# Performance work log

Measured on AMD Instinct MI355X. Metric: run time of the kernel, lower is better.

## Reference

```python
import jax, jax.numpy as jnp
import numpy as np

R = 16
SEQ_LEN = 96
D_MODEL = 512
D_FF = 2048


def tr_linear(x2d, in_cores, out_cores, bias):
    # Tensor-ring linear: W[i1..im, o1..on] = Tr(G1[i1]...Gm[im] H1[o1]...Hn[on])
    # y = x @ W.reshape(prod(in), prod(out)) + bias, computed without forming W fully.
    b = x2d.shape[0]
    in_dims = tuple(c.shape[1] for c in in_cores)
    t = x2d.reshape((b,) + in_dims)
    # fold input modes into the ring: s ends as [b, r0, r_m]
    s = jnp.tensordot(t, in_cores[0], axes=[[1], [1]])  # [b, i2..im, r0, r1]
    for core in in_cores[1:]:
        s = jnp.einsum('bi...ac,cid->b...ad', s, core)
    # fold output cores into W: [r_m, o1..on, r0]
    W = out_cores[0]
    for core in out_cores[1:]:
        W = jnp.einsum('c...d,dpe->c...pe', W, core)
    # close the ring: trace over (r0, r_m)
    y = jnp.einsum('bac,c...a->b...', s, W)
    return y.reshape(b, -1) + bias


def ffn_forward(x, c1_in2, c1_in3, c1_ind, c1_out_seq, c1_out_ff, b1,
                c2_in_seq, c2_in_ff, c2_out2, c2_out3, c2_outd, b2):
    B, L, D = x.shape
    in1 = list(c1_in2) + [c1_in3, c1_ind]          # factorint(96)+[d_model] modes
    out1 = [c1_out_seq, c1_out_ff]                 # [seq_len, d_ff]
    h = tr_linear(x.reshape(B, L * D), in1, out1, b1)   # [B, seq_len*d_ff]
    h = jax.nn.relu(h)                             # dropout = identity (eval mode)
    in2 = [c2_in_seq, c2_in_ff]
    out2 = list(c2_out2) + [c2_out3, c2_outd]
    y = tr_linear(h, in2, out2, b2)                # [B, seq_len*d_model]
    return y.reshape(B, L, D)                      # output.view(x.shape)


def setup_inputs():
    key = jax.random.key(0)
    ks = jax.random.split(key, 13)
    s = 0.2  # core init scale keeps 9-core ring products near unit magnitude
    return {
        'x': jax.random.normal(ks[0], (64, SEQ_LEN, D_MODEL), jnp.float32),
        'c1_in2': s * jax.random.normal(ks[1], (5, R, 2, R), jnp.float32),
        'c1_in3': s * jax.random.normal(ks[2], (R, 3, R), jnp.float32),
        'c1_ind': s * jax.random.normal(ks[3], (R, D_MODEL, R), jnp.float32),
        'c1_out_seq': s * jax.random.normal(ks[4], (R, SEQ_LEN, R), jnp.float32),
        'c1_out_ff': s * jax.random.normal(ks[5], (R, D_FF, R), jnp.float32),
        'b1': 0.01 * jax.random.normal(ks[6], (SEQ_LEN * D_FF,), jnp.float32),
        'c2_in_seq': s * jax.random.normal(ks[7], (R, SEQ_LEN, R), jnp.float32),
        'c2_in_ff': s * jax.random.normal(ks[8], (R, D_FF, R), jnp.float32),
        'c2_out2': s * jax.random.normal(ks[9], (5, R, 2, R), jnp.float32),
        'c2_out3': s * jax.random.normal(ks[10], (R, 3, R), jnp.float32),
        'c2_outd': s * jax.random.normal(ks[11], (R, D_MODEL, R), jnp.float32),
        'b2': 0.01 * jax.random.normal(ks[12], (SEQ_LEN * D_MODEL,), jnp.float32),
    }


def reference(x, c1_in2, c1_in3, c1_ind, c1_out_seq, c1_out_ff, b1,
              c2_in_seq, c2_in_ff, c2_out2, c2_out3, c2_outd, b2):
    return ffn_forward(x, c1_in2, c1_in3, c1_ind, c1_out_seq, c1_out_ff, b1,
                       c2_in_seq, c2_in_ff, c2_out2, c2_out3, c2_outd, b2)
```

## Files before the change

### kernel.cpp

```cpp
#include <hip/hip_runtime.h>


typedef _Float16 f16;
typedef f16 f16x8 __attribute__((ext_vector_type(8)));
typedef f16 f16x4 __attribute__((ext_vector_type(4)));
typedef float f32x4 __attribute__((ext_vector_type(4)));

__global__ void build_chain_kernel(
    const float* __restrict__ a5, const float* __restrict__ a3,
    const float* __restrict__ b5, const float* __restrict__ b3,
    float* __restrict__ Pout, float* __restrict__ Qout)
{
    __shared__ float bufA[8192];
    __shared__ float bufB[4096];
    const float* cores5 = (blockIdx.x == 0) ? a5 : b5;
    const float* core3  = (blockIdx.x == 0) ? a3 : b3;
    float* out = (blockIdx.x == 0) ? Pout : Qout;
    const int tid = threadIdx.x;

    for (int i = tid; i < 512; i += 256) bufA[i] = cores5[i];
    __syncthreads();

    float* prev = bufA; float* next = bufB;
    int m = 2;
    for (int g = 1; g < 5; ++g) {
        const float* G = cores5 + g * 512;
        const int mnew = m * 2;
        const int total = 256 * mnew;
        for (int idx = tid; idx < total; idx += 256) {
            const int rn = idx & 15;
            const int mm = (idx >> 4) % mnew;
            const int r0 = idx / (mnew * 16);
            const int mp = mm >> 1, i = mm & 1;
            float acc = 0.f;
            #pragma unroll
            for (int r = 0; r < 16; ++r)
                acc += prev[(r0 * m + mp) * 16 + r] * G[r * 32 + i * 16 + rn];
            next[idx] = acc;
        }
        __syncthreads();
        float* t = prev; prev = next; next = t;
        m = mnew;
    }
    {
        const int mnew = m * 3;
        const int total = 256 * mnew;
        for (int idx = tid; idx < total; idx += 256) {
            const int rn = idx & 15;
            const int mm = (idx >> 4) % mnew;
            const int r0 = idx / (mnew * 16);
            const int mp = mm / 3, i = mm % 3;
            float acc = 0.f;
            #pragma unroll
            for (int r = 0; r < 16; ++r)
                acc += prev[(r0 * m + mp) * 16 + r] * core3[r * 48 + i * 16 + rn];
            out[idx] = acc;
        }
    }
}

__global__ void permM_kernel(const float* __restrict__ in, f16* __restrict__ bh,
                             f16* __restrict__ bl, int K) {
    __shared__ float t[4096];
    const int q = blockIdx.x, k0 = blockIdx.y * 256;
    const float* src = in + ((size_t)q * K + k0) * 16;
    for (int i = threadIdx.x; i < 1024; i += 256)
        ((float4*)t)[i] = ((const float4*)src)[i];
    __syncthreads();
    const int j = threadIdx.x >> 4, kc = (threadIdx.x & 15) * 16;
    f16* dh = bh + (size_t)(q * 16 + j) * K + k0 + kc;
    f16* dl = bl + (size_t)(q * 16 + j) * K + k0 + kc;
    f16 vh[16], vl[16];
    #pragma unroll
    for (int i = 0; i < 16; ++i) {
        const float v = t[(kc + i) * 16 + j];
        const f16 h = (f16)v;
        vh[i] = h; vl[i] = (f16)(v - (float)h);
    }
    *(f16x8*)(dh) = *(f16x8*)&vh[0]; *(f16x8*)(dh + 8) = *(f16x8*)&vh[8];
    *(f16x8*)(dl) = *(f16x8*)&vl[0]; *(f16x8*)(dl + 8) = *(f16x8*)&vl[8];
}
__global__ void permO_kernel(const float* __restrict__ in, f16* __restrict__ bh,
                             f16* __restrict__ bl, int N) {
    const int idx = blockIdx.x * 256 + threadIdx.x;
    const int n = idx >> 8, k = idx & 255;
    const float v = in[((k >> 4) * N + n) * 16 + (k & 15)];
    const f16 h = (f16)v;
    bh[idx] = h; bl[idx] = (f16)(v - (float)h);
}

__global__ void xsplit_kernel(const float* __restrict__ x, f16* __restrict__ xh,
                              f16* __restrict__ xl) {
    const int idx = blockIdx.x * 256 + threadIdx.x;
    const float4 v = ((const float4*)x)[idx];
    f16x4 hh, ll;
    hh[0] = (f16)v.x; hh[1] = (f16)v.y; hh[2] = (f16)v.z; hh[3] = (f16)v.w;
    ll[0] = (f16)(v.x - (float)hh[0]); ll[1] = (f16)(v.y - (float)hh[1]);
    ll[2] = (f16)(v.z - (float)hh[2]); ll[3] = (f16)(v.w - (float)hh[3]);
    ((f16x4*)xh)[idx] = hh; ((f16x4*)xl)[idx] = ll;
}

__global__ void sfold_kernel(const float* __restrict__ z, const float* __restrict__ P,
                             float* __restrict__ spart, int SK) {
    const int b = blockIdx.x, lc = blockIdx.y, tid = threadIdx.x;
    const int r0 = tid >> 4, rE = tid & 15;
    float acc = 0.f;
    for (int sk = 0; sk < SK; ++sk) {
        const float* zb = z + ((size_t)sk * 6144 + b * 96) * 256;
        for (int l = lc * 16; l < lc * 16 + 16; ++l) {
            const float* zl = zb + l * 256 + rE;
            const float* Pl = P + (r0 * 96 + l) * 16;
            #pragma unroll
            for (int r = 0; r < 16; ++r) acc += zl[r * 16] * Pl[r];
        }
    }
    spart[((size_t)lc * 64 + b) * 256 + tid] = acc;
}

__global__ void uexpand_kernel(const float* __restrict__ spart, const float* __restrict__ O,
                               f16* __restrict__ uh, f16* __restrict__ ul) {
    __shared__ float s_sh[256], o_sh[256];
    const int o1 = blockIdx.x, b = blockIdx.y, tid = threadIdx.x;
    float sv = 0.f;
    #pragma unroll
    for (int lc = 0; lc < 6; ++lc) sv += spart[((size_t)lc * 64 + b) * 256 + tid];
    s_sh[tid] = sv;
    o_sh[tid] = O[((tid >> 4) * 96 + o1) * 16 + (tid & 15)];
    __syncthreads();
    const int dd = tid >> 4, a = tid & 15;
    float acc = 0.f;
    #pragma unroll
    for (int c = 0; c < 16; ++c) acc += s_sh[a * 16 + c] * o_sh[c * 16 + dd];
    const f16 h = (f16)acc;
    const size_t o = ((size_t)b * 96 + o1) * 256 + tid;
    uh[o] = h; ul[o] = (f16)(acc - (float)h);
}

template<int EPI>
__global__ __launch_bounds__(256) void trgemm_kernel(
    const f16* __restrict__ Ah, const f16* __restrict__ Al,
    const f16* __restrict__ BTh, const f16* __restrict__ BTl,
    const float* __restrict__ bias,
    float* __restrict__ Cf, f16* __restrict__ Ch, f16* __restrict__ Cl,
    int M, int N, int K, int kchunk)
{
    __shared__ f16 As[2][4 * 512];
    __shared__ f16 Bs[2][8 * 512];
    const int n0 = blockIdx.x * 128, m0 = blockIdx.y * 64;
    const int kbase = blockIdx.z * kchunk;
    const int tid = threadIdx.x;
    const int w = tid >> 6, lane = tid & 63;

    const int ar = tid >> 2, aq = tid & 3;
    const int bn = tid >> 1, bsg = tid & 1;
    const size_t a_off = (size_t)(m0 + ar) * K + kbase + aq * 8;
    const size_t b_off = (size_t)(n0 + bn) * K + kbase + bsg * 16;
    const int a_w = (ar >> 4) * 512 + aq * 128 + (ar & 15) * 8;
    const int b_w = (bn >> 4) * 512 + (bsg * 2) * 128 + (bn & 15) * 8;

    f32x4 acc[4][2];
    #pragma unroll
    for (int i = 0; i < 4; ++i) { acc[i][0] = (f32x4)0.f; acc[i][1] = (f32x4)0.f; }

    const int nkt = kchunk >> 5;
    for (int kt = 0; kt < nkt; ++kt) {
        const size_t ao = a_off + (size_t)kt * 32;
        const size_t bo = b_off + (size_t)kt * 32;
        const f16x8 avh = *(const f16x8*)(Ah + ao);
        const f16x8 avl = *(const f16x8*)(Al + ao);
        const f16x8 bvh0 = *(const f16x8*)(BTh + bo);
        const f16x8 bvh1 = *(const f16x8*)(BTh + bo + 8);
        const f16x8 bvl0 = *(const f16x8*)(BTl + bo);
        const f16x8 bvl1 = *(const f16x8*)(BTl + bo + 8);
        __syncthreads();
        *(f16x8*)&As[0][a_w] = avh;
        *(f16x8*)&As[1][a_w] = avl;
        *(f16x8*)&Bs[0][b_w] = bvh0;
        *(f16x8*)&Bs[0][b_w + 128] = bvh1;
        *(f16x8*)&Bs[1][b_w] = bvl0;
        *(f16x8*)&Bs[1][b_w + 128] = bvl1;
        __syncthreads();
        f16x8 afh[4], afl[4], bfh[2], bfl[2];
        #pragma unroll
        for (int mf = 0; mf < 4; ++mf) {
            afh[mf] = *(const f16x8*)&As[0][mf * 512 + lane * 8];
            afl[mf] = *(const f16x8*)&As[1][mf * 512 + lane * 8];
        }
        #pragma unroll
        for (int nf = 0; nf < 2; ++nf) {
            bfh[nf] = *(const f16x8*)&Bs[0][(w * 2 + nf) * 512 + lane * 8];
            bfl[nf] = *(const f16x8*)&Bs[1][(w * 2 + nf) * 512 + lane * 8];
        }
        #pragma unroll
        for (int mf = 0; mf < 4; ++mf)
            #pragma unroll
            for (int nf = 0; nf < 2; ++nf) {
                acc[mf][nf] = __builtin_amdgcn_mfma_f32_16x16x32_f16(afh[mf], bfh[nf], acc[mf][nf], 0, 0, 0);
                acc[mf][nf] = __builtin_amdgcn_mfma_f32_16x16x32_f16(afh[mf], bfl[nf], acc[mf][nf], 0, 0, 0);
                acc[mf][nf] = __builtin_amdgcn_mfma_f32_16x16x32_f16(afl[mf], bfh[nf], acc[mf][nf], 0, 0, 0);
            }
    }

    const int g = lane >> 4, c = lane & 15;
    #pragma unroll
    for (int mf = 0; mf < 4; ++mf)
        #pragma unroll
        for (int nf = 0; nf < 2; ++nf)
            #pragma unroll
            for (int r = 0; r < 4; ++r) {
                const int row = m0 + mf * 16 + g * 4 + r;
                const int col = n0 + w * 32 + nf * 16 + c;
                float v = acc[mf][nf][r];
                if constexpr (EPI == 0) {
                    Cf[((size_t)blockIdx.z * M + row) * N + col] = v;
                } else {
                    v += bias[(row % 96) * N + col];
                    if constexpr (EPI == 1) {
                        v = fmaxf(v, 0.f);
                        const f16 h = (f16)v;
                        Ch[(size_t)row * N + col] = h;
                        Cl[(size_t)row * N + col] = (f16)(v - (float)h);
                    } else {
                        Cf[(size_t)row * N + col] = v;
                    }
                }
            }
}

extern "C" void kernel_launch(void* const* d_in, const int* in_sizes, int n_in,
                              void* d_out, int out_size, void* d_ws, size_t ws_size,
                              hipStream_t stream) {
    const float* x        = (const float*)d_in[0];
    const float* c1_in2   = (const float*)d_in[1];
    const float* c1_in3   = (const float*)d_in[2];
    const float* c1_ind   = (const float*)d_in[3];
    const float* c1_oseq  = (const float*)d_in[4];
    const float* c1_off   = (const float*)d_in[5];
    const float* b1       = (const float*)d_in[6];
    const float* c2_iseq  = (const float*)d_in[7];
    const float* c2_iff   = (const float*)d_in[8];
    const float* c2_out2  = (const float*)d_in[9];
    const float* c2_out3  = (const float*)d_in[10];
    const float* c2_outd  = (const float*)d_in[11];
    const float* b2       = (const float*)d_in[12];
    float* out = (float*)d_out;

    float* wsf = (float*)d_ws;
    float* Pseq1 = wsf;
    float* Qseq2 = Pseq1 + 24576;
    float* spart = Qseq2 + 24576;
    float* zp    = spart + 98304;
    f16* fb   = (f16*)(zp + 2 * 6144 * 256);
    f16* BT1h = fb;
    f16* BT1l = BT1h + 131072;
    f16* BT2h = BT1l + 131072;
    f16* BT2l = BT2h + 524288;
    f16* BT3h = BT2l + 524288;
    f16* BT3l = BT3h + 524288;
    f16* BT4h = BT3l + 524288;
    f16* BT4l = BT4h + 131072;
    f16* uh   = BT4l + 131072;
    f16* ul   = uh + 1572864;
    f16* hh   = ul + 1572864;
    f16* hl   = hh + 12582912;
    f16* xh   = hh;
    f16* xl   = hh + 3145728;

    build_chain_kernel<<<2, 256, 0, stream>>>(c1_in2, c1_in3, c2_out2, c2_out3, Pseq1, Qseq2);
    permM_kernel<<<dim3(16, 2), 256, 0, stream>>>(c1_ind, BT1h, BT1l, 512);
    permO_kernel<<<2048, 256, 0, stream>>>(c1_off, BT2h, BT2l, 2048);
    permM_kernel<<<dim3(16, 8), 256, 0, stream>>>(c2_iff, BT3h, BT3l, 2048);
    permO_kernel<<<512, 256, 0, stream>>>(c2_outd, BT4h, BT4l, 512);
    xsplit_kernel<<<3072, 256, 0, stream>>>(x, xh, xl);

    trgemm_kernel<0><<<dim3(2, 96, 2), 256, 0, stream>>>(xh, xl, BT1h, BT1l, nullptr,
                                                         zp, nullptr, nullptr, 6144, 256, 512, 256);
    sfold_kernel<<<dim3(64, 6), 256, 0, stream>>>(zp, Pseq1, spart, 2);
    uexpand_kernel<<<dim3(96, 64), 256, 0, stream>>>(spart, c1_oseq, uh, ul);
    trgemm_kernel<1><<<dim3(16, 96, 1), 256, 0, stream>>>(uh, ul, BT2h, BT2l, b1,
                                                          nullptr, hh, hl, 6144, 2048, 256, 256);
    trgemm_kernel<0><<<dim3(2, 96, 2), 256, 0, stream>>>(hh, hl, BT3h, BT3l, nullptr,
                                                         zp, nullptr, nullptr, 6144, 256, 2048, 1024);
    sfold_kernel<<<dim3(64, 6), 256, 0, stream>>>(zp, c2_iseq, spart, 2);
    uexpand_kernel<<<dim3(96, 64), 256, 0, stream>>>(spart, Qseq2, uh, ul);
    trgemm_kernel<2><<<dim3(4, 96, 1), 256, 0, stream>>>(uh, ul, BT4h, BT4l, b2,
                                                         out, nullptr, nullptr, 6144, 512, 256, 256);
}
```

Before: 270.5 us.

## Rework TR-FFN pipeline: larger GEMM tiles, direct LDS loads, fused prep kernels

The GEMM moves from 64x128 to 128x128 block tiles with a 64-wide k step, loads tiles with global_load_lds straight into shared memory, and declares launch bounds of 256 threads with 2 blocks per CU. The chain-building kernel is parallelised across 192 blocks (one per sequence index) instead of 2. The four weight-permute kernels are merged into one launch. sfold now stages z and P in shared memory. Split-K rises to 4 when the workspace is large enough. Larger tiles give each block more data reuse but also launch fewer blocks and raise register and LDS pressure.

```diff
diff --git a/kernel.cpp b/kernel.cpp
--- a/kernel.cpp
+++ b/kernel.cpp
@@ -6,63 +6,45 @@
 typedef f16 f16x4 __attribute__((ext_vector_type(4)));
 typedef float f32x4 __attribute__((ext_vector_type(4)));
 
-__global__ void build_chain_kernel(
-    const float* __restrict__ a5, const float* __restrict__ a3,
-    const float* __restrict__ b5, const float* __restrict__ b3,
-    float* __restrict__ Pout, float* __restrict__ Qout)
-{
-    __shared__ float bufA[8192];
-    __shared__ float bufB[4096];
-    const float* cores5 = (blockIdx.x == 0) ? a5 : b5;
-    const float* core3  = (blockIdx.x == 0) ? a3 : b3;
-    float* out = (blockIdx.x == 0) ? Pout : Qout;
-    const int tid = threadIdx.x;
-
-    for (int i = tid; i < 512; i += 256) bufA[i] = cores5[i];
+__device__ __forceinline__ void gload16(const void* g, void* l) {
+    __builtin_amdgcn_global_load_lds(
+        (const __attribute__((address_space(1))) void*)g,
+        (__attribute__((address_space(3))) void*)l, 16, 0, 0);
+}
+
+__global__ void build_chain2_kernel(const float* __restrict__ a5, const float* __restrict__ a3,
+                                    const float* __restrict__ b5, const float* __restrict__ b3,
+                                    float* __restrict__ Pout, float* __restrict__ Qout) {
+    __shared__ float Ma[256], Mb[256];
+    const int l = blockIdx.x % 96, chain = blockIdx.x / 96;
+    const float* G5 = chain ? b5 : a5;
+    const float* G3 = chain ? b3 : a3;
+    float* out = chain ? Qout : Pout;
+    const int i6 = l % 3, lh = l / 3;
+    const int dig[5] = {(lh >> 4) & 1, (lh >> 3) & 1, (lh >> 2) & 1, (lh >> 1) & 1, lh & 1};
+    const int a = threadIdx.x >> 4, bn = threadIdx.x & 15;
+    Ma[threadIdx.x] = G5[a * 32 + dig[0] * 16 + bn];
     __syncthreads();
-
-    float* prev = bufA; float* next = bufB;
-    int m = 2;
+    float* cur = Ma; float* nxt = Mb;
     for (int g = 1; g < 5; ++g) {
-        const float* G = cores5 + g * 512;
-        const int mnew = m * 2;
-        const int total = 256 * mnew;
-        for (int idx = tid; idx < total; idx += 256) {
-            const int rn = idx & 15;
-            const int mm = (idx >> 4) % mnew;
-            const int r0 = idx / (mnew * 16);
-            const int mp = mm >> 1, i = mm & 1;
-            float acc = 0.f;
-            #pragma unroll
-            for (int r = 0; r < 16; ++r)
-                acc += prev[(r0 * m + mp) * 16 + r] * G[r * 32 + i * 16 + rn];
-            next[idx] = acc;
-        }
-        __syncthreads();
-        float* t = prev; prev = next; next = t;
-        m = mnew;
-    }
-    {
-        const int mnew = m * 3;
-        const int total = 256 * mnew;
-        for (int idx = tid; idx < total; idx += 256) {
-            const int rn = idx & 15;
-            const int mm = (idx >> 4) % mnew;
-            const int r0 = idx / (mnew * 16);
-            const int mp = mm / 3, i = mm % 3;
-            float acc = 0.f;
-            #pragma unroll
-            for (int r = 0; r < 16; ++r)
-                acc += prev[(r0 * m + mp) * 16 + r] * core3[r * 48 + i * 16 + rn];
-            out[idx] = acc;
-        }
-    }
-}
-
-__global__ void permM_kernel(const float* __restrict__ in, f16* __restrict__ bh,
-                             f16* __restrict__ bl, int K) {
-    __shared__ float t[4096];
-    const int q = blockIdx.x, k0 = blockIdx.y * 256;
+        float s = 0.f;
+        #pragma unroll
+        for (int r = 0; r < 16; ++r)
+            s += cur[a * 16 + r] * G5[g * 512 + r * 32 + dig[g] * 16 + bn];
+        nxt[threadIdx.x] = s;
+        __syncthreads();
+        float* t = cur; cur = nxt; nxt = t;
+    }
+    float s = 0.f;
+    #pragma unroll
+    for (int r = 0; r < 16; ++r)
+        s += cur[a * 16 + r] * G3[r * 48 + i6 * 16 + bn];
+    out[(a * 96 + l) * 16 + bn] = s;
+}
+
+__device__ __forceinline__ void permM_body(const float* __restrict__ in, f16* __restrict__ bh,
+                                           f16* __restrict__ bl, int K, int q, int k0,
+                                           float* t) {
     const float* src = in + ((size_t)q * K + k0) * 16;
     for (int i = threadIdx.x; i < 1024; i += 256)
         ((float4*)t)[i] = ((const float4*)src)[i];
@@ -80,13 +62,27 @@
     *(f16x8*)(dh) = *(f16x8*)&vh[0]; *(f16x8*)(dh + 8) = *(f16x8*)&vh[8];
     *(f16x8*)(dl) = *(f16x8*)&vl[0]; *(f16x8*)(dl + 8) = *(f16x8*)&vl[8];
 }
-__global__ void permO_kernel(const float* __restrict__ in, f16* __restrict__ bh,
-                             f16* __restrict__ bl, int N) {
-    const int idx = blockIdx.x * 256 + threadIdx.x;
+__device__ __forceinline__ void permO_body(const float* __restrict__ in, f16* __restrict__ bh,
+                                           f16* __restrict__ bl, int N, int blk) {
+    const int idx = blk * 256 + threadIdx.x;
     const int n = idx >> 8, k = idx & 255;
     const float v = in[((k >> 4) * N + n) * 16 + (k & 15)];
     const f16 h = (f16)v;
     bh[idx] = h; bl[idx] = (f16)(v - (float)h);
+}
+__global__ void prep_bt_kernel(const float* __restrict__ c1_ind, const float* __restrict__ c1_off,
+                               const float* __restrict__ c2_iff, const float* __restrict__ c2_outd,
+                               f16* BT1h, f16* BT1l, f16* BT2h, f16* BT2l,
+                               f16* BT3h, f16* BT3l, f16* BT4h, f16* BT4l) {
+    __shared__ float t[4096];
+    int b = blockIdx.x;
+    if (b < 32)   { permM_body(c1_ind, BT1h, BT1l, 512,  b & 15, (b >> 4) * 256, t); return; }
+    b -= 32;
+    if (b < 128)  { permM_body(c2_iff, BT3h, BT3l, 2048, b & 15, (b >> 4) * 256, t); return; }
+    b -= 128;
+    if (b < 2048) { permO_body(c1_off, BT2h, BT2l, 2048, b); return; }
+    b -= 2048;
+    permO_body(c2_outd, BT4h, BT4l, 512, b);
 }
 
 __global__ void xsplit_kernel(const float* __restrict__ x, f16* __restrict__ xh,
@@ -102,17 +98,25 @@
 
 __global__ void sfold_kernel(const float* __restrict__ z, const float* __restrict__ P,
                              float* __restrict__ spart, int SK) {
+    __shared__ float zs[4096];
+    __shared__ float Ps[4096];
     const int b = blockIdx.x, lc = blockIdx.y, tid = threadIdx.x;
     const int r0 = tid >> 4, rE = tid & 15;
+    for (int i = tid; i < 4096; i += 256) {
+        const int rp = i & 15, r = (i >> 4) & 15, l = i >> 8;
+        Ps[i] = P[((size_t)rp * 96 + lc * 16 + l) * 16 + r];
+    }
     float acc = 0.f;
     for (int sk = 0; sk < SK; ++sk) {
-        const float* zb = z + ((size_t)sk * 6144 + b * 96) * 256;
-        for (int l = lc * 16; l < lc * 16 + 16; ++l) {
-            const float* zl = zb + l * 256 + rE;
-            const float* Pl = P + (r0 * 96 + l) * 16;
-            #pragma unroll
-            for (int r = 0; r < 16; ++r) acc += zl[r * 16] * Pl[r];
-        }
+        const float4* zsrc = (const float4*)(z + ((size_t)sk * 6144 + b * 96 + lc * 16) * 256);
+        __syncthreads();
+        for (int i = tid; i < 1024; i += 256) ((float4*)zs)[i] = zsrc[i];
+        __syncthreads();
+        #pragma unroll
+        for (int l = 0; l < 16; ++l)
+            #pragma unroll
+            for (int r = 0; r < 16; ++r)
+                acc += zs[l * 256 + r * 16 + rE] * Ps[(l * 16 + r) * 16 + r0];
     }
     spart[((size_t)lc * 64 + b) * 256 + tid] = acc;
 }
@@ -137,84 +141,87 @@
 }
 
 template<int EPI>
-__global__ __launch_bounds__(256) void trgemm_kernel(
+__global__ __launch_bounds__(256, 2) void trgemm_kernel(
     const f16* __restrict__ Ah, const f16* __restrict__ Al,
     const f16* __restrict__ BTh, const f16* __restrict__ BTl,
     const float* __restrict__ bias,
     float* __restrict__ Cf, f16* __restrict__ Ch, f16* __restrict__ Cl,
     int M, int N, int K, int kchunk)
 {
-    __shared__ f16 As[2][4 * 512];
-    __shared__ f16 Bs[2][8 * 512];
-    const int n0 = blockIdx.x * 128, m0 = blockIdx.y * 64;
+    __shared__ f16 As[2][8192];
+    __shared__ f16 Bs[2][8192];
+    const int n0 = blockIdx.x * 128, m0 = blockIdx.y * 128;
     const int kbase = blockIdx.z * kchunk;
     const int tid = threadIdx.x;
     const int w = tid >> 6, lane = tid & 63;
-
-    const int ar = tid >> 2, aq = tid & 3;
-    const int bn = tid >> 1, bsg = tid & 1;
-    const size_t a_off = (size_t)(m0 + ar) * K + kbase + aq * 8;
-    const size_t b_off = (size_t)(n0 + bn) * K + kbase + bsg * 16;
-    const int a_w = (ar >> 4) * 512 + aq * 128 + (ar & 15) * 8;
-    const int b_w = (bn >> 4) * 512 + (bsg * 2) * 128 + (bn & 15) * 8;
-
-    f32x4 acc[4][2];
-    #pragma unroll
-    for (int i = 0; i < 4; ++i) { acc[i][0] = (f32x4)0.f; acc[i][1] = (f32x4)0.f; }
-
-    const int nkt = kchunk >> 5;
+    const int wm = w >> 1, wn = w & 1;
+    const int lr = lane & 15, lq = lane >> 4;
+
+    const int ra = 2 * w;
+    size_t aoff0 = (size_t)(m0 + ra * 16 + lr) * K + kbase + lq * 8;
+    size_t aoff1 = aoff0 + (size_t)16 * K;
+    size_t boff0 = (size_t)(n0 + ra * 16 + lr) * K + kbase + lq * 8;
+    size_t boff1 = boff0 + (size_t)16 * K;
+
+    f32x4 acc[4][4];
+    #pragma unroll
+    for (int i = 0; i < 4; ++i)
+        #pragma unroll
+        for (int j = 0; j < 4; ++j) acc[i][j] = (f32x4)0.f;
+
+    const int nkt = kchunk >> 6;
     for (int kt = 0; kt < nkt; ++kt) {
-        const size_t ao = a_off + (size_t)kt * 32;
-        const size_t bo = b_off + (size_t)kt * 32;
-        const f16x8 avh = *(const f16x8*)(Ah + ao);
-        const f16x8 avl = *(const f16x8*)(Al + ao);
-        const f16x8 bvh0 = *(const f16x8*)(BTh + bo);
-        const f16x8 bvh1 = *(const f16x8*)(BTh + bo + 8);
-        const f16x8 bvl0 = *(const f16x8*)(BTl + bo);
-        const f16x8 bvl1 = *(const f16x8*)(BTl + bo + 8);
-        __syncthreads();
-        *(f16x8*)&As[0][a_w] = avh;
-        *(f16x8*)&As[1][a_w] = avl;
-        *(f16x8*)&Bs[0][b_w] = bvh0;
-        *(f16x8*)&Bs[0][b_w + 128] = bvh1;
-        *(f16x8*)&Bs[1][b_w] = bvl0;
-        *(f16x8*)&Bs[1][b_w + 128] = bvl1;
-        __syncthreads();
-        f16x8 afh[4], afl[4], bfh[2], bfl[2];
-        #pragma unroll
-        for (int mf = 0; mf < 4; ++mf) {
-            afh[mf] = *(const f16x8*)&As[0][mf * 512 + lane * 8];
-            afl[mf] = *(const f16x8*)&As[1][mf * 512 + lane * 8];
+        __syncthreads();
+        #pragma unroll
+        for (int c = 0; c < 2; ++c) {
+            gload16(Ah + aoff0 + c * 32, &As[0][(ra + 0) * 1024 + c * 512]);
+            gload16(Ah + aoff1 + c * 32, &As[0][(ra + 1) * 1024 + c * 512]);
+            gload16(Al + aoff0 + c * 32, &As[1][(ra + 0) * 1024 + c * 512]);
+            gload16(Al + aoff1 + c * 32, &As[1][(ra + 1) * 1024 + c * 512]);
+            gload16(BTh + boff0 + c * 32, &Bs[0][(ra + 0) * 1024 + c * 512]);
+            gload16(BTh + boff1 + c * 32, &Bs[0][(ra + 1) * 1024 + c * 512]);
+            gload16(BTl + boff0 + c * 32, &Bs[1][(ra + 0) * 1024 + c * 512]);
+            gload16(BTl + boff1 + c * 32, &Bs[1][(ra + 1) * 1024 + c * 512]);
         }
-        #pragma unroll
-        for (int nf = 0; nf < 2; ++nf) {
-            bfh[nf] = *(const f16x8*)&Bs[0][(w * 2 + nf) * 512 + lane * 8];
-            bfl[nf] = *(const f16x8*)&Bs[1][(w * 2 + nf) * 512 + lane * 8];
+        aoff0 += 64; aoff1 += 64; boff0 += 64; boff1 += 64;
+        __syncthreads();
+        #pragma unroll
+        for (int ks = 0; ks < 2; ++ks) {
+            f16x8 afh[4], afl[4], bfh[4], bfl[4];
+            #pragma unroll
+            for (int mf = 0; mf < 4; ++mf) {
+                afh[mf] = *(const f16x8*)&As[0][(wm * 4 + mf) * 1024 + ks * 512 + lane * 8];
+                afl[mf] = *(const f16x8*)&As[1][(wm * 4 + mf) * 1024 + ks * 512 + lane * 8];
+            }
+            #pragma unroll
+            for (int nf = 0; nf < 4; ++nf) {
+                bfh[nf] = *(const f16x8*)&Bs[0][(wn * 4 + nf) * 1024 + ks * 512 + lane * 8];
+                bfl[nf] = *(const f16x8*)&Bs[1][(wn * 4 + nf) * 1024 + ks * 512 + lane * 8];
+            }
+            #pragma unroll
+            for (int mf = 0; mf < 4; ++mf)
+                #pragma unroll
+                for (int nf = 0; nf < 4; ++nf) {
+                    acc[mf][nf] = __builtin_amdgcn_mfma_f32_16x16x32_f16(afh[mf], bfh[nf], acc[mf][nf], 0, 0, 0);
+                    acc[mf][nf] = __builtin_amdgcn_mfma_f32_16x16x32_f16(afh[mf], bfl[nf], acc[mf][nf], 0, 0, 0);
+                    acc[mf][nf] = __builtin_amdgcn_mfma_f32_16x16x32_f16(afl[mf], bfh[nf], acc[mf][nf], 0, 0, 0);
+                }
         }
-        #pragma unroll
-        for (int mf = 0; mf < 4; ++mf)
-            #pragma unroll
-            for (int nf = 0; nf < 2; ++nf) {
-                acc[mf][nf] = __builtin_amdgcn_mfma_f32_16x16x32_f16(afh[mf], bfh[nf], acc[mf][nf], 0, 0, 0);
-                acc[mf][nf] = __builtin_amdgcn_mfma_f32_16x16x32_f16(afh[mf], bfl[nf], acc[mf][nf], 0, 0, 0);
-                acc[mf][nf] = __builtin_amdgcn_mfma_f32_16x16x32_f16(afl[mf], bfh[nf], acc[mf][nf], 0, 0, 0);
-            }
-    }
-
-    const int g = lane >> 4, c = lane & 15;
+    }
+
     #pragma unroll
     for (int mf = 0; mf < 4; ++mf)
         #pragma unroll
-        for (int nf = 0; nf < 2; ++nf)
+        for (int nf = 0; nf < 4; ++nf)
             #pragma unroll
             for (int r = 0; r < 4; ++r) {
-                const int row = m0 + mf * 16 + g * 4 + r;
-                const int col = n0 + w * 32 + nf * 16 + c;
+                const int row = m0 + wm * 64 + mf * 16 + lq * 4 + r;
+                const int col = n0 + wn * 64 + nf * 16 + lr;
                 float v = acc[mf][nf][r];
                 if constexpr (EPI == 0) {
                     Cf[((size_t)blockIdx.z * M + row) * N + col] = v;
                 } else {
-                    v += bias[(row % 96) * N + col];
+                    v += bias[(size_t)(row % 96) * N + col];
                     if constexpr (EPI == 1) {
                         v = fmaxf(v, 0.f);
                         const f16 h = (f16)v;
@@ -245,44 +252,46 @@
     const float* b2       = (const float*)d_in[12];
     float* out = (float*)d_out;
 
-    float* wsf = (float*)d_ws;
-    float* Pseq1 = wsf;
-    float* Qseq2 = Pseq1 + 24576;
-    float* spart = Qseq2 + 24576;
-    float* zp    = spart + 98304;
-    f16* fb   = (f16*)(zp + 2 * 6144 * 256);
-    f16* BT1h = fb;
-    f16* BT1l = BT1h + 131072;
-    f16* BT2h = BT1l + 131072;
-    f16* BT2l = BT2h + 524288;
-    f16* BT3h = BT2l + 524288;
-    f16* BT3l = BT3h + 524288;
-    f16* BT4h = BT3l + 524288;
-    f16* BT4l = BT4h + 131072;
-    f16* uh   = BT4l + 131072;
-    f16* ul   = uh + 1572864;
-    f16* hh   = ul + 1572864;
-    f16* hl   = hh + 12582912;
-    f16* xh   = hh;
-    f16* xl   = hh + 3145728;
-
-    build_chain_kernel<<<2, 256, 0, stream>>>(c1_in2, c1_in3, c2_out2, c2_out3, Pseq1, Qseq2);
-    permM_kernel<<<dim3(16, 2), 256, 0, stream>>>(c1_ind, BT1h, BT1l, 512);
-    permO_kernel<<<2048, 256, 0, stream>>>(c1_off, BT2h, BT2l, 2048);
-    permM_kernel<<<dim3(16, 8), 256, 0, stream>>>(c2_iff, BT3h, BT3l, 2048);
-    permO_kernel<<<512, 256, 0, stream>>>(c2_outd, BT4h, BT4l, 512);
+    char* base = (char*)d_ws;
+    float* Pseq1 = (float*)base;
+    float* Qseq2 = (float*)(base + 98304);
+    f16*   BT1h  = (f16*)(base + 196608);
+    f16*   BT1l  = BT1h + 131072;
+    f16*   BT2h  = BT1l + 131072;
+    f16*   BT2l  = BT2h + 524288;
+    f16*   BT3h  = BT2l + 524288;
+    f16*   BT3l  = BT3h + 524288;
+    f16*   BT4h  = BT3l + 524288;
+    f16*   BT4l  = BT4h + 131072;
+    char*  hreg  = base + 5439488;
+    f16*   hh    = (f16*)hreg;
+    f16*   hl    = hh + 12582912;
+    f16*   xh    = (f16*)hreg;
+    f16*   xl    = xh + 3145728;
+    float* spart = (float*)(hreg + 12582912);
+    char*  zreg  = base + 55771136;
+    float* zp    = (float*)zreg;
+    f16*   uh    = (f16*)zreg;
+    f16*   ul    = uh + 1572864;
+
+    const size_t need4 = 55771136 + 4ull * 6291456;
+    const int SK = (ws_size >= need4) ? 4 : 2;
+
+    build_chain2_kernel<<<192, 256, 0, stream>>>(c1_in2, c1_in3, c2_out2, c2_out3, Pseq1, Qseq2);
+    prep_bt_kernel<<<2720, 256, 0, stream>>>(c1_ind, c1_off, c2_iff, c2_outd,
+                                             BT1h, BT1l, BT2h, BT2l, BT3h, BT3l, BT4h, BT4l);
     xsplit_kernel<<<3072, 256, 0, stream>>>(x, xh, xl);
 
-    trgemm_kernel<0><<<dim3(2, 96, 2), 256, 0, stream>>>(xh, xl, BT1h, BT1l, nullptr,
-                                                         zp, nullptr, nullptr, 6144, 256, 512, 256);
-    sfold_kernel<<<dim3(64, 6), 256, 0, stream>>>(zp, Pseq1, spart, 2);
+    trgemm_kernel<0><<<dim3(2, 48, SK), 256, 0, stream>>>(xh, xl, BT1h, BT1l, nullptr,
+                                                          zp, nullptr, nullptr, 6144, 256, 512, 512 / SK);
+    sfold_kernel<<<dim3(64, 6), 256, 0, stream>>>(zp, Pseq1, spart, SK);
     uexpand_kernel<<<dim3(96, 64), 256, 0, stream>>>(spart, c1_oseq, uh, ul);
-    trgemm_kernel<1><<<dim3(16, 96, 1), 256, 0, stream>>>(uh, ul, BT2h, BT2l, b1,
+    trgemm_kernel<1><<<dim3(16, 48, 1), 256, 0, stream>>>(uh, ul, BT2h, BT2l, b1,
                                                           nullptr, hh, hl, 6144, 2048, 256, 256);
-    trgemm_kernel<0><<<dim3(2, 96, 2), 256, 0, stream>>>(hh, hl, BT3h, BT3l, nullptr,
-                                                         zp, nullptr, nullptr, 6144, 256, 2048, 1024);
-    sfold_kernel<<<dim3(64, 6), 256, 0, stream>>>(zp, c2_iseq, spart, 2);
+    trgemm_kernel<0><<<dim3(2, 48, SK), 256, 0, stream>>>(hh, hl, BT3h, BT3l, nullptr,
+                                                          zp, nullptr, nullptr, 6144, 256, 2048, 2048 / SK);
+    sfold_kernel<<<dim3(64, 6), 256, 0, stream>>>(zp, c2_iseq, spart, SK);
     uexpand_kernel<<<dim3(96, 64), 256, 0, stream>>>(spart, Qseq2, uh, ul);
-    trgemm_kernel<2><<<dim3(4, 96, 1), 256, 0, stream>>>(uh, ul, BT4h, BT4l, b2,
+    trgemm_kernel<2><<<dim3(4, 48, 1), 256, 0, stream>>>(uh, ul, BT4h, BT4l, b2,
                                                          out, nullptr, nullptr, 6144, 512, 256, 256);
 }
```

New measurement: 272.4 us. About the same (+0.7%).
